# Kernel tuning notes

Hardware: AMD Instinct MI355X
Metric: run time of the kernel (lower is better)

## Reference

```python
import jax, jax.numpy as jnp
import numpy as np

N_NODES = 100000
N_EDGES = 320000
N_GRAPHS = 4096
HID = 256
NUM_FEAT = 28


def setup_inputs() -> dict:
    key = jax.random.key(0)
    ks = jax.random.split(key, 20)
    inp = {}
    inp['x'] = jax.random.normal(ks[0], (N_NODES, NUM_FEAT), dtype=jnp.float32)
    inp['edge_index'] = jax.random.randint(ks[1], (2, N_EDGES), 0, N_NODES, dtype=jnp.int64)
    inp['batch'] = jnp.sort(jax.random.randint(ks[2], (N_NODES,), 0, N_GRAPHS, dtype=jnp.int64))
    def lin(k, out_d, in_d, scale=None):
        s = scale if scale is not None else 1.0 / np.sqrt(in_d)
        return jax.random.uniform(k, (out_d, in_d), jnp.float32, -s, s)
    # GraphConv layer l: W_rel (neighbor aggregate), b_rel, W_root (self)
    dims = [(HID, NUM_FEAT), (HID, HID), (HID, HID), (HID, HID)]
    for i, (o, d) in enumerate(dims, 1):
        inp[f'W{i}_rel'] = lin(ks[2 + 3 * i], o, d)
        inp[f'b{i}_rel'] = jnp.zeros((o,), jnp.float32)
        inp[f'W{i}_root'] = lin(ks[3 + 3 * i], o, d)
    inp['fc1_w'] = lin(ks[15], HID, 4 * HID)
    inp['fc1_b'] = jnp.zeros((HID,), jnp.float32)
    inp['fc2_w'] = lin(ks[16], HID, HID)
    inp['fc2_b'] = jnp.zeros((HID,), jnp.float32)
    inp['fc3_w'] = lin(ks[17], HID, HID)
    inp['fc3_b'] = jnp.zeros((HID,), jnp.float32)
    inp['fc4_w'] = lin(ks[18], 1, HID)
    inp['fc4_b'] = jnp.zeros((1,), jnp.float32)
    return inp


def _graph_conv(x, src, dst, W_rel, b_rel, W_root):
    # PyG GraphConv (aggr='add'): out = lin_rel(sum_{j->i} x_j) + lin_root(x_i)
    agg = jax.ops.segment_sum(x[src], dst, num_segments=N_NODES)  # [N, d]
    return agg @ W_rel.T + b_rel + x @ W_root.T


def reference(x, edge_index, batch,
              W1_rel, b1_rel, W1_root, W2_rel, b2_rel, W2_root,
              W3_rel, b3_rel, W3_root, W4_rel, b4_rel, W4_root,
              fc1_w, fc1_b, fc2_w, fc2_b, fc3_w, fc3_b, fc4_w, fc4_b):
    src, dst = edge_index[0], edge_index[1]
    x1 = jax.nn.relu(_graph_conv(x, src, dst, W1_rel, b1_rel, W1_root))
    x2 = jax.nn.relu(_graph_conv(x1, src, dst, W2_rel, b2_rel, W2_root))
    x3 = jax.nn.relu(_graph_conv(x2, src, dst, W3_rel, b3_rel, W3_root))
    x4 = jax.nn.relu(_graph_conv(x3, src, dst, W4_rel, b4_rel, W4_root))
    h = jnp.concatenate([x1, x2, x3, x4], axis=-1)  # [N, 4*HID]
    # global mean pool over graphs
    sums = jax.ops.segment_sum(h, batch, num_segments=N_GRAPHS)  # [G, 4*HID]
    cnts = jax.ops.segment_sum(jnp.ones((h.shape[0],), h.dtype), batch, num_segments=N_GRAPHS)
    g = sums / jnp.maximum(cnts, 1.0)[:, None]
    g = jax.nn.relu(g @ fc1_w.T + fc1_b)
    g = jax.nn.relu(g @ fc2_w.T + fc2_b)
    g = jax.nn.relu(g @ fc3_w.T + fc3_b)
    out = g @ fc4_w.T + fc4_b  # [G, 1]
    return out.reshape(-1)
```

## Files before the change

### kernel.cpp

```cpp
#include <hip/hip_runtime.h>
#include <hip/hip_bf16.h>
#include <cstdio>

#define HID 256

using short8  = __attribute__((ext_vector_type(8))) short;
using floatx4 = __attribute__((ext_vector_type(4))) float;

typedef const unsigned int __attribute__((address_space(1)))* as1_cuintp;
typedef unsigned int __attribute__((address_space(3)))* as3_uintp;

__device__ inline unsigned short bf16_rn(float x) {
    unsigned u = __float_as_uint(x);
    return (unsigned short)((u + 0x7FFFu + ((u >> 16) & 1u)) >> 16);
}
__device__ inline float bf2f(unsigned short u) {
    return __uint_as_float(((unsigned)u) << 16);
}

__global__ void marker_k(float* __restrict__ out, int n, float v) {
    int i = blockIdx.x * blockDim.x + threadIdx.x;
    if (i < n) out[i] = v;
}

__global__ void detect64_k(const unsigned* __restrict__ eiw, int E,
                           const unsigned* __restrict__ bw, int Nh,
                           int* __restrict__ any_nonzero) {
    int total = E + Nh;
    unsigned loc = 0;
    for (int i = blockIdx.x * blockDim.x + threadIdx.x; i < total;
         i += gridDim.x * blockDim.x) {
        loc |= (i < E) ? eiw[2 * i + 1] : bw[2 * (i - E) + 1];
    }
    if (loc) atomicOr(any_nonzero, 1);
}

__global__ void norm_idx_k(const int* __restrict__ src, int* __restrict__ dst,
                           int n, const int* __restrict__ any_nonzero) {
    int is64 = (any_nonzero[0] == 0);
    for (int i = blockIdx.x * blockDim.x + threadIdx.x; i < n;
         i += gridDim.x * blockDim.x) {
        dst[i] = is64 ? src[2 * i] : src[i];
    }
}

__global__ void pool_bounds_k(const int* __restrict__ batch, int N, int G,
                              int* __restrict__ starts) {
    int g = blockIdx.x * blockDim.x + threadIdx.x;
    if (g > G) return;
    int lo = 0, hi = N;
    while (lo < hi) {
        int mid = (lo + hi) >> 1;
        if (batch[mid] < g) lo = mid + 1; else hi = mid;
    }
    starts[g] = lo;
}

__global__ void deg_count_k(const int* __restrict__ ei, int E, int N,
                            int* __restrict__ deg) {
    int e = blockIdx.x * blockDim.x + threadIdx.x;
    if (e >= E) return;
    int s = ei[e];
    int d = ei[E + e];
    if ((unsigned)s >= (unsigned)N || (unsigned)d >= (unsigned)N) return;
    atomicAdd(&deg[d], 1);
}

#define SCAN_BLK 256

__global__ __launch_bounds__(SCAN_BLK) void scan_a_k(const int* __restrict__ deg,
                                                     int* __restrict__ bsum, int N) {
    __shared__ int red[SCAN_BLK];
    int i = blockIdx.x * SCAN_BLK + threadIdx.x;
    int v = (i < N) ? deg[i] : 0;
    red[threadIdx.x] = v;
    __syncthreads();
#pragma unroll
    for (int off = SCAN_BLK / 2; off > 0; off >>= 1) {
        if (threadIdx.x < off) red[threadIdx.x] += red[threadIdx.x + off];
        __syncthreads();
    }
    if (threadIdx.x == 0) bsum[blockIdx.x] = red[0];
}

__global__ __launch_bounds__(1024) void scan_b_k(int* __restrict__ bsum, int nb) {
    __shared__ int tsum[1024];
    int t = threadIdx.x;
    int v = (t < nb) ? bsum[t] : 0;
    tsum[t] = v;
    __syncthreads();
    for (int off = 1; off < 1024; off <<= 1) {
        int u = (t >= off) ? tsum[t - off] : 0;
        __syncthreads();
        tsum[t] += u;
        __syncthreads();
    }
    if (t < nb) bsum[t] = tsum[t] - v;
}

__global__ __launch_bounds__(SCAN_BLK) void scan_c_k(const int* __restrict__ deg,
                                                     const int* __restrict__ bsum,
                                                     int* __restrict__ row_ptr, int N) {
    __shared__ int tsum[SCAN_BLK];
    int t = threadIdx.x;
    int i = blockIdx.x * SCAN_BLK + t;
    int v = (i < N) ? deg[i] : 0;
    tsum[t] = v;
    __syncthreads();
    for (int off = 1; off < SCAN_BLK; off <<= 1) {
        int u = (t >= off) ? tsum[t - off] : 0;
        __syncthreads();
        tsum[t] += u;
        __syncthreads();
    }
    if (i <= N) row_ptr[i] = tsum[t] - v + bsum[blockIdx.x];
}

__global__ __launch_bounds__(1024) void scan_rowptr_k(const int* __restrict__ deg,
                                                      int* __restrict__ row_ptr, int N) {
    __shared__ int tsum[1024];
    int t = threadIdx.x;
    int chunk = (N + 1023) / 1024;
    int lo = t * chunk;
    int hi = min(lo + chunk, N);
    int s = 0;
    for (int i = lo; i < hi; i++) s += deg[i];
    tsum[t] = s;
    __syncthreads();
    for (int off = 1; off < 1024; off <<= 1) {
        int v = (t >= off) ? tsum[t - off] : 0;
        __syncthreads();
        tsum[t] += v;
        __syncthreads();
    }
    int run = (t == 0) ? 0 : tsum[t - 1];
    for (int i = lo; i < hi; i++) { row_ptr[i] = run; run += deg[i]; }
    if (hi >= N && lo <= N) row_ptr[N] = run;
}

__global__ void fill_csr_k(const int* __restrict__ ei, int E, int N,
                           const int* __restrict__ row_ptr, int* __restrict__ cursor,
                           int* __restrict__ esrc) {
    int e = blockIdx.x * blockDim.x + threadIdx.x;
    if (e >= E) return;
    int s = ei[e];
    int d = ei[E + e];
    if ((unsigned)s >= (unsigned)N || (unsigned)d >= (unsigned)N) return;
    int pos = atomicAdd(&cursor[d], 1);
    esrc[row_ptr[d] + pos] = s;
}

__global__ void gather28_k(const float* __restrict__ x, const int* __restrict__ row_ptr,
                           const int* __restrict__ esrc, float* __restrict__ Q28, int N) {
    int gid = blockIdx.x * blockDim.x + threadIdx.x;
    int node = gid >> 5;
    if (node >= N) return;
    int lane = gid & 31;
    if (lane >= 28) return;
    int s = row_ptr[node], e = row_ptr[node + 1];
    float acc = 0.f;
    for (int i = s; i < e; i++) {
        int src = esrc[i];
        acc += x[(size_t)src * 28 + lane];
    }
    Q28[(size_t)node * 28 + lane] = acc;
}

__global__ void gather256_k(const float* __restrict__ P, const int* __restrict__ row_ptr,
                            const int* __restrict__ esrc, float* __restrict__ Q, int N) {
    int gid = blockIdx.x * blockDim.x + threadIdx.x;
    int node = gid >> 6;
    if (node >= N) return;
    int lane = gid & 63;
    int s = row_ptr[node], e = row_ptr[node + 1];
    float4 acc = make_float4(0.f, 0.f, 0.f, 0.f);
    for (int i = s; i < e; i++) {
        int src = esrc[i];
        float4 v = *(const float4*)(P + (size_t)src * HID + lane * 4);
        acc.x += v.x; acc.y += v.y; acc.z += v.z; acc.w += v.w;
    }
    *(float4*)(Q + (size_t)node * HID + lane * 4) = acc;
}

__global__ __launch_bounds__(256) void l1_fused_k(
    const float* __restrict__ x, const float* __restrict__ agg,
    const float* __restrict__ Wrel, const float* __restrict__ Wroot,
    const float* __restrict__ bias, float* __restrict__ out, int M) {
    __shared__ float As[64][28];
    __shared__ float Xs[64][28];
    int t = threadIdx.x;
    int n0 = blockIdx.x * 64;
    float wrel[28], wroot[28];
#pragma unroll
    for (int k = 0; k < 28; k++) {
        wrel[k]  = Wrel[t * 28 + k];
        wroot[k] = Wroot[t * 28 + k];
    }
    float b = bias[t];
    for (int idx = t; idx < 64 * 28; idx += 256) {
        int r = idx / 28;
        int c = idx - r * 28;
        int gr = n0 + r;
        As[r][c] = (gr < M) ? agg[(size_t)gr * 28 + c] : 0.f;
        Xs[r][c] = (gr < M) ? x[(size_t)gr * 28 + c] : 0.f;
    }
    __syncthreads();
    int nmax = min(64, M - n0);
    for (int n = 0; n < nmax; n++) {
        float acc = b;
#pragma unroll
        for (int k4 = 0; k4 < 28; k4 += 4) {
            float4 a  = *(const float4*)&As[n][k4];
            float4 xx = *(const float4*)&Xs[n][k4];
            acc += a.x * wrel[k4] + a.y * wrel[k4 + 1] + a.z * wrel[k4 + 2] + a.w * wrel[k4 + 3];
            acc += xx.x * wroot[k4] + xx.y * wroot[k4 + 1] + xx.z * wroot[k4 + 2] + xx.w * wroot[k4 + 3];
        }
        out[(size_t)(n0 + n) * HID + t] = fmaxf(acc, 0.f);
    }
}

__global__ void wsplit6_k(const float* W0, const float* W1, const float* W2,
                          const float* W3, const float* W4, const float* W5,
                          unsigned short* __restrict__ out_hl, int n) {
    int i = blockIdx.x * blockDim.x + threadIdx.x;
    if (i >= n) return;
    const float* W = (blockIdx.y == 0) ? W0 : (blockIdx.y == 1) ? W1 :
                     (blockIdx.y == 2) ? W2 : (blockIdx.y == 3) ? W3 :
                     (blockIdx.y == 4) ? W4 : W5;
    unsigned short* o = out_hl + (size_t)blockIdx.y * 131072;
    float a = W[i];
    unsigned short h = bf16_rn(a);
    unsigned short lo = bf16_rn(a - bf2f(h));
    int col = i >> 8;
    int k   = i & 255;
    int ch  = k >> 5;
    int sg  = (k >> 3) & 3;
    int e   = k & 7;
    int gp  = sg ^ ((col >> 1) & 3);
    size_t base = (size_t)ch * 16384 + (size_t)col * 32 + gp * 8 + e;
    o[base] = h;
    o[base + 8192] = lo;
}

#define LSTR 40

__global__ __launch_bounds__(256) void gemm_strip_mfma_k(
    const float* __restrict__ Q, const unsigned short* __restrict__ Wr_hl,
    float* __restrict__ P, const unsigned short* __restrict__ Wo_hl,
    const float* __restrict__ bias, int M) {
    __shared__ __attribute__((aligned(16))) unsigned short Ah[64 * LSTR];
    __shared__ __attribute__((aligned(16))) unsigned short Al[64 * LSTR];
    __shared__ __attribute__((aligned(16))) unsigned short Wbuf[8192];
    int t = threadIdx.x;
    int brow = blockIdx.x * 64;
    int w = t >> 6;
    int l = t & 63;

    floatx4 acc[4][4];
#pragma unroll
    for (int i = 0; i < 4; i++)
#pragma unroll
        for (int j = 0; j < 4; j++) acc[i][j] = (floatx4){0.f, 0.f, 0.f, 0.f};

    int srow = t >> 2;
    int sg   = t & 3;

    for (int ch = 0; ch < 16; ch++) {
        int phase2 = (ch >= 8);
        const float* A = phase2 ? P : Q;
        const unsigned short* Whl = phase2 ? Wo_hl : Wr_hl;
        int kbase = (ch & 7) * 32;

        {
            const char* wg = (const char*)(Whl + (size_t)(ch & 7) * 16384) + w * 4096;
            char* ld = (char*)Wbuf + w * 4096;
#pragma unroll
            for (int i = 0; i < 4; i++) {
                __builtin_amdgcn_global_load_lds(
                    (as1_cuintp)(const void*)(wg + i * 1024 + l * 16),
                    (as3_uintp)(void*)(ld + i * 1024),
                    16, 0, 0);
            }
        }
        {
            int gr = brow + srow;
            float v[8];
            if (gr < M) {
                float4 u0 = *(const float4*)(A + (size_t)gr * HID + kbase + sg * 8);
                float4 u1 = *(const float4*)(A + (size_t)gr * HID + kbase + sg * 8 + 4);
                v[0] = u0.x; v[1] = u0.y; v[2] = u0.z; v[3] = u0.w;
                v[4] = u1.x; v[5] = u1.y; v[6] = u1.z; v[7] = u1.w;
            } else {
#pragma unroll
                for (int j = 0; j < 8; j++) v[j] = 0.f;
            }
            union { unsigned short us[8]; short8 v8; } hh, ll;
#pragma unroll
            for (int j = 0; j < 8; j++) {
                unsigned short h = bf16_rn(v[j]);
                float hf = __uint_as_float(((unsigned)h) << 16);
                hh.us[j] = h;
                ll.us[j] = bf16_rn(v[j] - hf);
            }
            int base = srow * LSTR + sg * 8;
            *(short8*)(Ah + base) = hh.v8;
            *(short8*)(Al + base) = ll.v8;
        }
        __syncthreads();

        int frow = l & 15;
        int fg   = l >> 4;
        short8 ahf[4], alf[4], wf[4];
#pragma unroll
        for (int rt = 0; rt < 4; rt++) {
            int base = (rt * 16 + frow) * LSTR + fg * 8;
            ahf[rt] = *(short8*)(Ah + base);
            alf[rt] = *(short8*)(Al + base);
        }
#pragma unroll
        for (int ct = 0; ct < 4; ct++) {
            int col = w * 64 + ct * 16 + frow;
            int gp = fg ^ ((col >> 1) & 3);
            wf[ct] = *(short8*)(Wbuf + col * 32 + gp * 8);
        }
        asm volatile("s_waitcnt lgkmcnt(0)" ::: "memory");
        __builtin_amdgcn_sched_barrier(0);
        {
            const char* wg = (const char*)(Whl + (size_t)(ch & 7) * 16384 + 8192) + w * 4096;
            char* ld = (char*)Wbuf + w * 4096;
#pragma unroll
            for (int i = 0; i < 4; i++) {
                __builtin_amdgcn_global_load_lds(
                    (as1_cuintp)(const void*)(wg + i * 1024 + l * 16),
                    (as3_uintp)(void*)(ld + i * 1024),
                    16, 0, 0);
            }
        }
#pragma unroll
        for (int rt = 0; rt < 4; rt++)
#pragma unroll
            for (int ct = 0; ct < 4; ct++) {
                acc[rt][ct] = __builtin_amdgcn_mfma_f32_16x16x32_bf16(
                    ahf[rt], wf[ct], acc[rt][ct], 0, 0, 0);
                acc[rt][ct] = __builtin_amdgcn_mfma_f32_16x16x32_bf16(
                    alf[rt], wf[ct], acc[rt][ct], 0, 0, 0);
            }
        asm volatile("s_waitcnt vmcnt(0)" ::: "memory");
        __builtin_amdgcn_sched_barrier(0);
#pragma unroll
        for (int ct = 0; ct < 4; ct++) {
            int col = w * 64 + ct * 16 + frow;
            int gp = fg ^ ((col >> 1) & 3);
            wf[ct] = *(short8*)(Wbuf + col * 32 + gp * 8);
        }
#pragma unroll
        for (int rt = 0; rt < 4; rt++)
#pragma unroll
            for (int ct = 0; ct < 4; ct++)
                acc[rt][ct] = __builtin_amdgcn_mfma_f32_16x16x32_bf16(
                    ahf[rt], wf[ct], acc[rt][ct], 0, 0, 0);
        __syncthreads();
    }

#pragma unroll
    for (int ct = 0; ct < 4; ct++) {
        int gc = w * 64 + ct * 16 + (l & 15);
        float bs = bias[gc];
#pragma unroll
        for (int rt = 0; rt < 4; rt++) {
            floatx4 a = acc[rt][ct];
#pragma unroll
            for (int r = 0; r < 4; r++) {
                int gr = brow + rt * 16 + (l >> 4) * 4 + r;
                if (gr < M)
                    P[(size_t)gr * HID + gc] = fmaxf(a[r] + bs, 0.f);
            }
        }
    }
}

__global__ __launch_bounds__(256) void pool_slice_k(const float* __restrict__ xl,
                                                    const int* __restrict__ starts,
                                                    float* __restrict__ gslice, int N) {
    int g = blockIdx.x;
    int t = threadIdx.x;
    int s = starts[g], e = starts[g + 1];
    s = max(0, min(s, N));
    e = max(s, min(e, N));
    float a = 0.f;
    for (int n = s; n < e; n++) a += xl[(size_t)n * HID + t];
    float inv = 1.f / (float)max(e - s, 1);
    gslice[(size_t)g * 1024 + t] = a * inv;
}

#define BM 64
#define BN 64
#define BK 32
#define LP 68

__global__ __launch_bounds__(256) void gemm_dual_k(
    const float* __restrict__ A1, int lda1, const float* __restrict__ W1,
    const float* __restrict__ A2, int lda2, const float* __restrict__ W2,
    const float* __restrict__ bias, float* __restrict__ out, int ldout,
    int M, int K1, int K2, int relu) {
    __shared__ float As[BK][LP];
    __shared__ float Ws[BK][LP];
    int t = threadIdx.x;
    int brow = blockIdx.x * BM;
    int bcol = blockIdx.y * BN;
    int tx = t & 15, ty = t >> 4;
    float acc[4][4] = {{0.f}};
    int Ktot = K1 + K2;
    int srow = t >> 3;
    int sk4 = (t & 7) << 2;

    for (int kk = 0; kk < Ktot; kk += BK) {
        int phase2 = (kk >= K1);
        const float* A = phase2 ? A2 : A1;
        const float* W = phase2 ? W2 : W1;
        int lda = phase2 ? lda2 : lda1;
        int ldw = phase2 ? K2 : K1;
        int kbase = phase2 ? (kk - K1) : kk;
#pragma unroll
        for (int i = 0; i < 2; i++) {
            int r = srow + i * 32;
            int gr = brow + r;
            float4 v = make_float4(0.f, 0.f, 0.f, 0.f);
            if (gr < M) v = *(const float4*)(A + (size_t)gr * lda + kbase + sk4);
            As[sk4 + 0][r] = v.x; As[sk4 + 1][r] = v.y;
            As[sk4 + 2][r] = v.z; As[sk4 + 3][r] = v.w;
            float4 w = *(const float4*)(W + (size_t)(bcol + r) * ldw + kbase + sk4);
            Ws[sk4 + 0][r] = w.x; Ws[sk4 + 1][r] = w.y;
            Ws[sk4 + 2][r] = w.z; Ws[sk4 + 3][r] = w.w;
        }
        __syncthreads();
#pragma unroll
        for (int k = 0; k < BK; k++) {
            float4 a = *(const float4*)&As[k][ty << 2];
            float4 w = *(const float4*)&Ws[k][tx << 2];
            float av[4] = {a.x, a.y, a.z, a.w};
            float wv[4] = {w.x, w.y, w.z, w.w};
#pragma unroll
            for (int i = 0; i < 4; i++)
#pragma unroll
                for (int j = 0; j < 4; j++)
                    acc[i][j] = fmaf(av[i], wv[j], acc[i][j]);
        }
        __syncthreads();
    }
#pragma unroll
    for (int i = 0; i < 4; i++) {
        int gr = brow + (ty << 2) + i;
        if (gr >= M) continue;
#pragma unroll
        for (int j = 0; j < 4; j++) {
            int gc = bcol + (tx << 2) + j;
            float v = acc[i][j] + bias[gc];
            if (relu) v = fmaxf(v, 0.f);
            out[(size_t)gr * ldout + gc] = v;
        }
    }
}

__global__ void fc4_k(const float* __restrict__ in, const float* __restrict__ w,
                      const float* __restrict__ b, float* __restrict__ out, int M) {
    int gid = blockIdx.x * blockDim.x + threadIdx.x;
    int row = gid >> 6;
    if (row >= M) return;
    int lane = gid & 63;
    float4 v  = *(const float4*)(in + (size_t)row * HID + lane * 4);
    float4 ww = *(const float4*)(w + lane * 4);
    float acc = v.x * ww.x + v.y * ww.y + v.z * ww.z + v.w * ww.w;
#pragma unroll
    for (int off = 32; off; off >>= 1) acc += __shfl_down(acc, off);
    if (lane == 0) out[row] = acc + b[0];
}

extern "C" void kernel_launch(void* const* d_in, const int* in_sizes, int n_in,
                              void* d_out, int out_size, void* d_ws, size_t ws_size,
                              hipStream_t stream) {
    const int N = in_sizes[0] / 28;
    const int E = in_sizes[1] / 2;
    const int G = out_size;

    const float* x        = (const float*)d_in[0];
    const int*   ei_raw   = (const int*)d_in[1];
    const int*   b_raw    = (const int*)d_in[2];
    const float* W1_rel  = (const float*)d_in[3];
    const float* b1      = (const float*)d_in[4];
    const float* W1_root = (const float*)d_in[5];
    const float* W2_rel  = (const float*)d_in[6];
    const float* b2      = (const float*)d_in[7];
    const float* W2_root = (const float*)d_in[8];
    const float* W3_rel  = (const float*)d_in[9];
    const float* b3      = (const float*)d_in[10];
    const float* W3_root = (const float*)d_in[11];
    const float* W4_rel  = (const float*)d_in[12];
    const float* b4      = (const float*)d_in[13];
    const float* W4_root = (const float*)d_in[14];
    const float* fc1_w = (const float*)d_in[15];
    const float* fc1_b = (const float*)d_in[16];
    const float* fc2_w = (const float*)d_in[17];
    const float* fc2_b = (const float*)d_in[18];
    const float* fc3_w = (const float*)d_in[19];
    const float* fc3_b = (const float*)d_in[20];
    const float* fc4_w = (const float*)d_in[21];
    const float* fc4_b = (const float*)d_in[22];
    float* out = (float*)d_out;

    size_t fN  = (size_t)N * HID;
    size_t off_P      = 0;
    size_t off_Q      = off_P + fN;
    size_t off_gpool  = off_Q + fN;
    size_t off_t1     = off_gpool + (size_t)G * 1024;
    size_t off_t2     = off_t1 + (size_t)G * HID;
    size_t off_ei     = off_t2 + (size_t)G * HID;
    size_t off_batch  = off_ei + (size_t)2 * E;
    size_t off_starts = off_batch + (size_t)N;
    size_t off_flag   = off_starts + (size_t)(G + 1);
    size_t off_deg    = off_flag + 1;
    size_t off_cur    = off_deg + (size_t)N;
    size_t off_rowp   = off_cur + (size_t)N;
    size_t off_bsum   = off_rowp + (size_t)(N + 1);
    size_t off_esrc   = off_bsum + 1024;
    size_t off_wsplit = (off_esrc + (size_t)E + 3) & ~(size_t)3;
    size_t need = (off_wsplit + 393216 + 16) * 4;

    if (ws_size < need) {
        fprintf(stderr, "[kernel_launch] ws too small: ws=%zu need=%zu\n", ws_size, need);
        marker_k<<<(G + 255) / 256, 256, 0, stream>>>(out, G, (float)(ws_size >> 20));
        return;
    }

    float* wsf   = (float*)d_ws;
    float* P     = wsf + off_P;
    float* Q     = wsf + off_Q;
    float* gpool = wsf + off_gpool;
    float* t1    = wsf + off_t1;
    float* t2    = wsf + off_t2;
    int* nei     = (int*)(wsf + off_ei);
    int* nbatch  = (int*)(wsf + off_batch);
    int* starts  = (int*)(wsf + off_starts);
    int* flag    = (int*)(wsf + off_flag);
    int* deg     = (int*)(wsf + off_deg);
    int* cursor  = (int*)(wsf + off_cur);
    int* row_ptr = (int*)(wsf + off_rowp);
    int* bsum    = (int*)(wsf + off_bsum);
    int* esrc    = (int*)(wsf + off_esrc);
    unsigned short* wsplit = (unsigned short*)(wsf + off_wsplit);

    hipMemsetAsync(flag, 0, sizeof(int), stream);
    detect64_k<<<1024, 256, 0, stream>>>((const unsigned*)ei_raw, E,
                                         (const unsigned*)b_raw, N / 2, flag);
    norm_idx_k<<<1024, 256, 0, stream>>>(ei_raw, nei, 2 * E, flag);
    norm_idx_k<<<512, 256, 0, stream>>>(b_raw, nbatch, N, flag);

    pool_bounds_k<<<(G + 1 + 255) / 256, 256, 0, stream>>>(nbatch, N, G, starts);

    hipMemsetAsync(deg, 0, 2 * (size_t)N * sizeof(int), stream);
    deg_count_k<<<(E + 255) / 256, 256, 0, stream>>>(nei, E, N, deg);
    int nb = (N + 1 + SCAN_BLK - 1) / SCAN_BLK;
    if (nb <= 1024) {
        scan_a_k<<<nb, SCAN_BLK, 0, stream>>>(deg, bsum, N);
        scan_b_k<<<1, 1024, 0, stream>>>(bsum, nb);
        scan_c_k<<<nb, SCAN_BLK, 0, stream>>>(deg, bsum, row_ptr, N);
    } else {
        scan_rowptr_k<<<1, 1024, 0, stream>>>(deg, row_ptr, N);
    }
    fill_csr_k<<<(E + 255) / 256, 256, 0, stream>>>(nei, E, N, row_ptr, cursor, esrc);

    wsplit6_k<<<dim3((65536 + 255) / 256, 6), 256, 0, stream>>>(
        W2_rel, W2_root, W3_rel, W3_root, W4_rel, W4_root, wsplit, 65536);

    int nstrips = (N + 63) / 64;

    gather28_k<<<((size_t)N * 32 + 255) / 256, 256, 0, stream>>>(x, row_ptr, esrc, Q, N);
    l1_fused_k<<<nstrips, 256, 0, stream>>>(x, Q, W1_rel, W1_root, b1, P, N);
    pool_slice_k<<<G, 256, 0, stream>>>(P, starts, gpool + 0, N);

    const float* bb[3] = {b2, b3, b4};
    for (int l = 0; l < 3; l++) {
        gather256_k<<<((size_t)N * 64 + 255) / 256, 256, 0, stream>>>(P, row_ptr, esrc, Q, N);
        gemm_strip_mfma_k<<<nstrips, 256, 0, stream>>>(
            Q, wsplit + (size_t)(2 * l) * 131072,
            P, wsplit + (size_t)(2 * l + 1) * 131072, bb[l], N);
        pool_slice_k<<<G, 256, 0, stream>>>(P, starts, gpool + 256 * (l + 1), N);
    }

    dim3 gdimG(G / BM, HID / BN);
    gemm_dual_k<<<gdimG, 256, 0, stream>>>(gpool, 1024, fc1_w, nullptr, 0, nullptr,
                                           fc1_b, t1, HID, G, 1024, 0, 1);
    gemm_dual_k<<<gdimG, 256, 0, stream>>>(t1, HID, fc2_w, nullptr, 0, nullptr,
                                           fc2_b, t2, HID, G, HID, 0, 1);
    gemm_dual_k<<<gdimG, 256, 0, stream>>>(t2, HID, fc3_w, nullptr, 0, nullptr,
                                           fc3_b, t1, HID, G, HID, 0, 1);
    fc4_k<<<(G * 64 + 255) / 256, 256, 0, stream>>>(t1, fc4_w, fc4_b, out, G);
}
```

Before: 970.9 us.

## Fuse neighbor gather into the MFMA GraphConv GEMM with ping-pong buffers

Removes the separate gather256 kernel and its intermediate Q buffer. The strip GEMM now sums neighbor rows from CSR directly while staging each 32-wide K chunk of the relation phase. It ping-pongs the input and output activation buffers, since the fused kernel reads neighbor rows of the previous layer while writing the new one. This saves writing and re-reading an N x 256 float buffer per layer, but the irregular neighbor loads now sit on the GEMM's critical path and are split into 8 separate chunk passes with narrower per-thread loads.

```diff
diff --git a/kernel.cpp b/kernel.cpp
--- a/kernel.cpp
+++ b/kernel.cpp
@@ -164,22 +164,6 @@
         acc += x[(size_t)src * 28 + lane];
     }
     Q28[(size_t)node * 28 + lane] = acc;
-}
-
-__global__ void gather256_k(const float* __restrict__ P, const int* __restrict__ row_ptr,
-                            const int* __restrict__ esrc, float* __restrict__ Q, int N) {
-    int gid = blockIdx.x * blockDim.x + threadIdx.x;
-    int node = gid >> 6;
-    if (node >= N) return;
-    int lane = gid & 63;
-    int s = row_ptr[node], e = row_ptr[node + 1];
-    float4 acc = make_float4(0.f, 0.f, 0.f, 0.f);
-    for (int i = s; i < e; i++) {
-        int src = esrc[i];
-        float4 v = *(const float4*)(P + (size_t)src * HID + lane * 4);
-        acc.x += v.x; acc.y += v.y; acc.z += v.z; acc.w += v.w;
-    }
-    *(float4*)(Q + (size_t)node * HID + lane * 4) = acc;
 }
 
 __global__ __launch_bounds__(256) void l1_fused_k(
@@ -244,9 +228,10 @@
 
 #define LSTR 40
 
-__global__ __launch_bounds__(256) void gemm_strip_mfma_k(
-    const float* __restrict__ Q, const unsigned short* __restrict__ Wr_hl,
-    float* __restrict__ P, const unsigned short* __restrict__ Wo_hl,
+__global__ __launch_bounds__(256) void gemm_fused_k(
+    const int* __restrict__ row_ptr, const int* __restrict__ esrc,
+    const float* __restrict__ Pin, const unsigned short* __restrict__ Wr_hl,
+    float* __restrict__ Pout, const unsigned short* __restrict__ Wo_hl,
     const float* __restrict__ bias, int M) {
     __shared__ __attribute__((aligned(16))) unsigned short Ah[64 * LSTR];
     __shared__ __attribute__((aligned(16))) unsigned short Al[64 * LSTR];
@@ -264,10 +249,12 @@
 
     int srow = t >> 2;
     int sg   = t & 3;
+    int gr   = brow + srow;
+    int es = 0, ee = 0;
+    if (gr < M) { es = row_ptr[gr]; ee = row_ptr[gr + 1]; }
 
     for (int ch = 0; ch < 16; ch++) {
         int phase2 = (ch >= 8);
-        const float* A = phase2 ? P : Q;
         const unsigned short* Whl = phase2 ? Wo_hl : Wr_hl;
         int kbase = (ch & 7) * 32;
 
@@ -283,16 +270,24 @@
             }
         }
         {
-            int gr = brow + srow;
-            float v[8];
+            float v[8] = {0.f, 0.f, 0.f, 0.f, 0.f, 0.f, 0.f, 0.f};
             if (gr < M) {
-                float4 u0 = *(const float4*)(A + (size_t)gr * HID + kbase + sg * 8);
-                float4 u1 = *(const float4*)(A + (size_t)gr * HID + kbase + sg * 8 + 4);
-                v[0] = u0.x; v[1] = u0.y; v[2] = u0.z; v[3] = u0.w;
-                v[4] = u1.x; v[5] = u1.y; v[6] = u1.z; v[7] = u1.w;
-            } else {
-#pragma unroll
-                for (int j = 0; j < 8; j++) v[j] = 0.f;
+                if (!phase2) {
+                    for (int i = es; i < ee; i++) {
+                        int src = esrc[i];
+                        const float* pr = Pin + (size_t)src * HID + kbase + sg * 8;
+                        float4 u0 = *(const float4*)pr;
+                        float4 u1 = *(const float4*)(pr + 4);
+                        v[0] += u0.x; v[1] += u0.y; v[2] += u0.z; v[3] += u0.w;
+                        v[4] += u1.x; v[5] += u1.y; v[6] += u1.z; v[7] += u1.w;
+                    }
+                } else {
+                    const float* pr = Pin + (size_t)gr * HID + kbase + sg * 8;
+                    float4 u0 = *(const float4*)pr;
+                    float4 u1 = *(const float4*)(pr + 4);
+                    v[0] = u0.x; v[1] = u0.y; v[2] = u0.z; v[3] = u0.w;
+                    v[4] = u1.x; v[5] = u1.y; v[6] = u1.z; v[7] = u1.w;
+                }
             }
             union { unsigned short us[8]; short8 v8; } hh, ll;
 #pragma unroll
@@ -371,9 +366,9 @@
             floatx4 a = acc[rt][ct];
 #pragma unroll
             for (int r = 0; r < 4; r++) {
-                int gr = brow + rt * 16 + (l >> 4) * 4 + r;
-                if (gr < M)
-                    P[(size_t)gr * HID + gc] = fmaxf(a[r] + bs, 0.f);
+                int orow = brow + rt * 16 + (l >> 4) * 4 + r;
+                if (orow < M)
+                    Pout[(size_t)orow * HID + gc] = fmaxf(a[r] + bs, 0.f);
             }
         }
     }
@@ -509,9 +504,9 @@
     float* out = (float*)d_out;
 
     size_t fN  = (size_t)N * HID;
-    size_t off_P      = 0;
-    size_t off_Q      = off_P + fN;
-    size_t off_gpool  = off_Q + fN;
+    size_t off_P0     = 0;
+    size_t off_P1     = off_P0 + fN;
+    size_t off_gpool  = off_P1 + fN;
     size_t off_t1     = off_gpool + (size_t)G * 1024;
     size_t off_t2     = off_t1 + (size_t)G * HID;
     size_t off_ei     = off_t2 + (size_t)G * HID;
@@ -533,8 +528,8 @@
     }
 
     float* wsf   = (float*)d_ws;
-    float* P     = wsf + off_P;
-    float* Q     = wsf + off_Q;
+    float* P0    = wsf + off_P0;
+    float* P1    = wsf + off_P1;
     float* gpool = wsf + off_gpool;
     float* t1    = wsf + off_t1;
     float* t2    = wsf + off_t2;
@@ -574,17 +569,19 @@
 
     int nstrips = (N + 63) / 64;
 
-    gather28_k<<<((size_t)N * 32 + 255) / 256, 256, 0, stream>>>(x, row_ptr, esrc, Q, N);
-    l1_fused_k<<<nstrips, 256, 0, stream>>>(x, Q, W1_rel, W1_root, b1, P, N);
-    pool_slice_k<<<G, 256, 0, stream>>>(P, starts, gpool + 0, N);
+    gather28_k<<<((size_t)N * 32 + 255) / 256, 256, 0, stream>>>(x, row_ptr, esrc, P1, N);
+    l1_fused_k<<<nstrips, 256, 0, stream>>>(x, P1, W1_rel, W1_root, b1, P0, N);
+    pool_slice_k<<<G, 256, 0, stream>>>(P0, starts, gpool + 0, N);
 
     const float* bb[3] = {b2, b3, b4};
+    float* bufs[2] = {P0, P1};
     for (int l = 0; l < 3; l++) {
-        gather256_k<<<((size_t)N * 64 + 255) / 256, 256, 0, stream>>>(P, row_ptr, esrc, Q, N);
-        gemm_strip_mfma_k<<<nstrips, 256, 0, stream>>>(
-            Q, wsplit + (size_t)(2 * l) * 131072,
-            P, wsplit + (size_t)(2 * l + 1) * 131072, bb[l], N);
-        pool_slice_k<<<G, 256, 0, stream>>>(P, starts, gpool + 256 * (l + 1), N);
+        float* Pin  = bufs[l & 1];
+        float* Pout = bufs[(l + 1) & 1];
+        gemm_fused_k<<<nstrips, 256, 0, stream>>>(
+            row_ptr, esrc, Pin, wsplit + (size_t)(2 * l) * 131072,
+            Pout, wsplit + (size_t)(2 * l + 1) * 131072, bb[l], N);
+        pool_slice_k<<<G, 256, 0, stream>>>(Pout, starts, gpool + 256 * (l + 1), N);
     }
 
     dim3 gdimG(G / BM, HID / BN);
```

Result: slower. 1.053 ms (+8.5%).
